# Kernel optimization log

Hardware: AMD Instinct MI355X
Metric: run time of the kernel (lower is better)

## Reference

```python
import jax, jax.numpy as jnp
import numpy as np

ALPHA = 0.2        # LeakyReLU negative slope
NEG_INF = -9e15    # mask value used by the torch module


def setup_inputs() -> dict:
    key = jax.random.key(0)
    ks = jax.random.split(key, 7)
    B, T, N, Cin = 4, 12, 1024, 64
    Fout, Em = 64, 16
    x = jax.random.normal(ks[0], (B, T, N, Cin), dtype=jnp.float32)
    adj = jax.random.randint(ks[1], (N, N), 0, 2, dtype=jnp.int32)
    emb1 = jax.random.normal(ks[2], (N, Em), dtype=jnp.float32)
    emb2 = jax.random.normal(ks[3], (N, Em), dtype=jnp.float32)
    W = jax.random.normal(ks[4], (Cin, Fout), dtype=jnp.float32) * (1.0 / np.sqrt(Cin))
    a = jax.random.normal(ks[5], (2 * Fout, 1), dtype=jnp.float32) * 0.1
    a2 = jax.random.normal(ks[6], (2 * Em, 1), dtype=jnp.float32) * 0.1
    return {"x": x, "adj": adj, "emb1": emb1, "emb2": emb2, "W": W, "a": a, "a2": a2}


def reference(x, adj, emb1, emb2, W, a, a2):
    B, T, N, Cin = x.shape
    Fout = W.shape[1]
    Em = emb1.shape[1]
    # Linear projection, fold batch*time: Wh [BT, N, Fout]
    Wh = jnp.einsum('btnc,cf->btnf', x, W).reshape(B * T, N, Fout)
    # Additive attention scores from node features
    s1 = Wh @ a[:Fout, 0]          # [BT, N]
    s2 = Wh @ a[Fout:, 0]          # [BT, N]
    e1 = s1[:, :, None] + s2[:, None, :]   # [BT, N, N]
    # Additive scores from static embeddings (shared across batch*time)
    f1 = emb1 @ a2[:Em, 0]         # [N]
    f2 = emb2 @ a2[Em:, 0]         # [N]
    e2 = f1[:, None] + f2[None, :]          # [N, N]
    e = jax.nn.leaky_relu(e1 + e2[None, :, :], negative_slope=ALPHA)
    # Adjacency mask + row softmax (dropout is inference no-op)
    att = jnp.where(adj[None, :, :] > 0, e, jnp.float32(NEG_INF))
    att = jax.nn.softmax(att, axis=-1)
    h_prime = att @ Wh                       # [BT, N, Fout]
    return jax.nn.elu(h_prime.reshape(B, T, N, Fout))
```

## Files before the change

kernel.cpp:

```cpp
#include <hip/hip_runtime.h>
#include <hip/hip_bf16.h>
#include <math.h>

#define BT 48
#define N 1024
#define F 64
#define CIN 64
#define EM 16
#define LRELU_A 0.2f
#define L2E 1.4426950408889634f

typedef short bf16x8 __attribute__((ext_vector_type(8)));
typedef float f32x4  __attribute__((ext_vector_type(4)));
typedef unsigned int u32x4 __attribute__((ext_vector_type(4)));

__device__ __forceinline__ unsigned short f2bf(float f) {
    unsigned int u = __float_as_uint(f);
    return (unsigned short)((u + 0x7FFFu + ((u >> 16) & 1u)) >> 16);
}

__global__ __launch_bounds__(256) void k_proj_misc(
    const float* __restrict__ x, const float* __restrict__ W,
    const float* __restrict__ a,
    const int* __restrict__ adj,
    const float* __restrict__ emb1, const float* __restrict__ emb2,
    const float* __restrict__ a2,
    unsigned short* __restrict__ WhSw,
    float* __restrict__ s1, float* __restrict__ s2,
    unsigned int* __restrict__ adjBits,
    float* __restrict__ f1, float* __restrict__ f2)
{
    const int tid = threadIdx.x;
    const int b   = blockIdx.x;

    __shared__ __align__(16) float sx[64 * 64];
    __shared__ __align__(16) float sWT[64 * 68];
    __shared__ __align__(16) unsigned short sT[64 * 80];

    const int bt  = b >> 4;
    const int n0  = (b & 15) * 64;
    const size_t grow = (size_t)bt * N + n0;

    {
        const float4* xv = (const float4*)(x + grow * CIN);
        float4* sxv = (float4*)sx;
        for (int i = tid; i < 64 * CIN / 4; i += 256) sxv[i] = xv[i];
        for (int i = tid; i < CIN * F; i += 256)
            sWT[(i & 63) * 68 + (i >> 6)] = W[i];
    }
    __syncthreads();

    const int f = tid & 63;
    const int w = tid >> 6;
    const float a1 = a[f], a2c = a[F + f];

    float acc[16];
#pragma unroll
    for (int t = 0; t < 16; ++t) acc[t] = 0.f;

    for (int cb = 0; cb < CIN; cb += 4) {
        const float4 wv = *(const float4*)&sWT[f * 68 + cb];
#pragma unroll
        for (int t = 0; t < 16; ++t) {
            const float4 xv = *(const float4*)&sx[(w * 16 + t) * 64 + cb];
            acc[t] = fmaf(xv.x, wv.x, acc[t]);
            acc[t] = fmaf(xv.y, wv.y, acc[t]);
            acc[t] = fmaf(xv.z, wv.z, acc[t]);
            acc[t] = fmaf(xv.w, wv.w, acc[t]);
        }
    }

#pragma unroll
    for (int t = 0; t < 16; ++t) {
        float v1 = acc[t] * a1;
        float v2 = acc[t] * a2c;
#pragma unroll
        for (int off = 32; off >= 1; off >>= 1) {
            v1 += __shfl_xor(v1, off, 64);
            v2 += __shfl_xor(v2, off, 64);
        }
        if (f == 0) {
            s1[grow + w * 16 + t] = v1;
            s2[grow + w * 16 + t] = v2;
        }
        sT[f * 80 + w * 16 + t] = f2bf(acc[t]);
    }
    __syncthreads();

    {
        const int ff = tid >> 2, q = tid & 3;
        const int slot = (q + ff) & 3;
        const int nb0 = (b & 15) * 2;
#pragma unroll
        for (int nbL = 0; nbL < 2; ++nbL) {
            const size_t dst = ((size_t)(bt * 32 + nb0 + nbL) * 64 + ff) * 32 + slot * 8;
            *(uint4*)&WhSw[dst] = *(const uint4*)&sT[ff * 80 + nbL * 32 + q * 8];
        }
    }

    if (b < 128) {
        const int idx = b * 256 + tid;
        const int r = idx >> 5, w32 = idx & 31;
        const int* p = adj + (size_t)r * N + w32 * 32;
        unsigned int m = 0;
#pragma unroll
        for (int j = 0; j < 32; ++j) m |= (p[j] > 0 ? 1u : 0u) << j;
        adjBits[idx] = m;
    } else if (b < 132) {
        const int n = (b - 128) * 256 + tid;
        float v1 = 0.f, v2 = 0.f;
#pragma unroll
        for (int k = 0; k < EM; ++k) {
            v1 = fmaf(emb1[n * EM + k], a2[k], v1);
            v2 = fmaf(emb2[n * EM + k], a2[EM + k], v2);
        }
        f1[n] = v1; f2[n] = v2;
    }
}


#define WAIT_VM4 asm volatile("s_waitcnt vmcnt(4)" ::: "memory")
#define WAIT_VM0 asm volatile("s_waitcnt vmcnt(0)" ::: "memory")
#define BAR __builtin_amdgcn_s_barrier()

#define PAIR(x1e, x1o, x2e, x2o, bit, dest) do {                           \
    float p0_ = fmaxf((x1e) * E1, (x2e) * E2);                             \
    float p1_ = fmaxf((x1o) * E1, (x2o) * E2);                             \
    p0_ = ((mb_ >> (bit)) & 1u) ? p0_ : 0.f;                               \
    p1_ = ((mb_ >> ((bit) + 1)) & 1u) ? p1_ : 0.f;                         \
    lsum += p0_ + p1_;                                                     \
    unsigned int pk_;                                                      \
    asm("v_cvt_pk_bf16_f32 %0, %1, %2" : "=v"(pk_) : "v"(p0_), "v"(p1_)); \
    dest = pk_;                                                            \
} while (0)

#define MAKE_ONE(ch, ks, Avar, abword) do {                                \
    const int jb_ = (ch) * 128 + (ks) * 32 + q * 8;                        \
    const float4 x1a_ = *(const float4*)&sX1[jb_];                         \
    const float4 x1b_ = *(const float4*)&sX1[jb_ + 4];                     \
    const float4 x2a_ = *(const float4*)&sX2[jb_];                         \
    const float4 x2b_ = *(const float4*)&sX2[jb_ + 4];                     \
    const unsigned int mb_ = ((abword) >> (q * 8)) & 0xFFu;                \
    unsigned int u0_, u1_, u2_, u3_;                                       \
    PAIR(x1a_.x, x1a_.y, x2a_.x, x2a_.y, 0, u0_);                          \
    PAIR(x1a_.z, x1a_.w, x2a_.z, x2a_.w, 2, u1_);                          \
    PAIR(x1b_.x, x1b_.y, x2b_.x, x2b_.y, 4, u2_);                          \
    PAIR(x1b_.z, x1b_.w, x2b_.z, x2b_.w, 6, u3_);                          \
    u32x4 av_; av_.x = u0_; av_.y = u1_; av_.z = u2_; av_.w = u3_;         \
    Avar = __builtin_bit_cast(bf16x8, av_);                                \
} while (0)

#define MAKE_AFR(ch, abv, A0, A1, A2, A3) do {                             \
    MAKE_ONE(ch, 0, A0, abv.x);                                            \
    MAKE_ONE(ch, 1, A1, abv.y);                                            \
    MAKE_ONE(ch, 2, A2, abv.z);                                            \
    MAKE_ONE(ch, 3, A3, abv.w);                                            \
} while (0)

#define MFMA_KS(ct, ks, Af) do {                                           \
    const bf16x8 bb_ = *(const bf16x8*)(src_ + (ks) * 4096 +               \
                        ((ct) * 16 + m15) * 64 + slotoff);                 \
    acc##ct = __builtin_amdgcn_mfma_f32_16x16x32_bf16(Af, bb_, acc##ct,    \
                                                      0, 0, 0);            \
} while (0)

#define MFMA_CT(ct, A0, A1, A2, A3) do {                                   \
    MFMA_KS(ct, 0, A0); MFMA_KS(ct, 1, A1);                                \
    MFMA_KS(ct, 2, A2); MFMA_KS(ct, 3, A3);                                \
} while (0)

#define MFMA_CHUNK(ch, A0, A1, A2, A3) do {                                \
    const char* src_ = (const char*)sB[(ch) & 1];                          \
    MFMA_CT(0, A0, A1, A2, A3); MFMA_CT(1, A0, A1, A2, A3);                \
    MFMA_CT(2, A0, A1, A2, A3); MFMA_CT(3, A0, A1, A2, A3);                \
} while (0)

#define DMA(ch) do {                                                       \
    const unsigned short* dsrc_ = gBbt + (ch) * 8192 + w * 2048 + lane * 8;\
    unsigned short* ddst_ = &sB[(ch) & 1][w * 2048];                       \
    __builtin_amdgcn_global_load_lds(                                      \
        (const __attribute__((address_space(1))) unsigned int*)(dsrc_),    \
        (__attribute__((address_space(3))) unsigned int*)(ddst_), 16, 0, 0);\
    __builtin_amdgcn_global_load_lds(                                      \
        (const __attribute__((address_space(1))) unsigned int*)(dsrc_+512),\
        (__attribute__((address_space(3))) unsigned int*)(ddst_+512), 16, 0, 0);\
    __builtin_amdgcn_global_load_lds(                                      \
        (const __attribute__((address_space(1))) unsigned int*)(dsrc_+1024),\
        (__attribute__((address_space(3))) unsigned int*)(ddst_+1024), 16, 0, 0);\
    __builtin_amdgcn_global_load_lds(                                      \
        (const __attribute__((address_space(1))) unsigned int*)(dsrc_+1536),\
        (__attribute__((address_space(3))) unsigned int*)(ddst_+1536), 16, 0, 0);\
} while (0)

#define EPI(ct, accv) do {                                                 \
    float h0_ = accv.x * rinv0, h1_ = accv.y * rinv1,                      \
          h2_ = accv.z * rinv2, h3_ = accv.w * rinv3;                      \
    h0_ = (h0_ > 0.f) ? h0_ : (__expf(h0_) - 1.f);                         \
    h1_ = (h1_ > 0.f) ? h1_ : (__expf(h1_) - 1.f);                         \
    h2_ = (h2_ > 0.f) ? h2_ : (__expf(h2_) - 1.f);                         \
    h3_ = (h3_ > 0.f) ? h3_ : (__expf(h3_) - 1.f);                         \
    float* op_ = out + (size_t)(bt * N + i0 + w * 16 + q * 4) * F          \
                 + (ct) * 16 + m15;                                        \
    op_[0 * F] = h0_; op_[1 * F] = h1_; op_[2 * F] = h2_; op_[3 * F] = h3_;\
} while (0)

__global__ __launch_bounds__(256, 3) void k_attn(
    const unsigned int* __restrict__ adjBits,
    const unsigned short* __restrict__ WhSw,
    const float* __restrict__ s1, const float* __restrict__ s2,
    const float* __restrict__ f1v, const float* __restrict__ f2v,
    float* __restrict__ out)
{
    __shared__ __align__(16) float sX1[N];
    __shared__ __align__(16) float sX2[N];
    __shared__ __align__(16) unsigned short sB[2][8192];
    __shared__ float sWmax[4];

    const int tid  = threadIdx.x;
    const int xcd = blockIdx.x & 7;
    const int idx = blockIdx.x >> 3;
    const int bt  = xcd * 6 + (idx >> 4);
    const int i0  = (idx & 15) * 64;
    const int lane = tid & 63;
    const int w    = tid >> 6;
    const int q    = lane >> 4;
    const int m15  = lane & 15;

    const int growq = i0 + w * 16 + m15;
    const unsigned int* abRow = adjBits + growq * 32;
    const uint4* abRow4 = (const uint4*)abRow;

    const uint4 ab0 = abRow4[0], ab1 = abRow4[1], ab2 = abRow4[2], ab3 = abRow4[3];
    const uint4 ab4 = abRow4[4], ab5 = abRow4[5], ab6 = abRow4[6], ab7 = abRow4[7];
    const float rraw = s1[bt * N + growq] + f1v[growq];

    float cmax = -1e30f;
    for (int j = tid; j < N; j += 256) {
        const float c = (s2[bt * N + j] + f2v[j]) * L2E;
        sX1[j] = exp2f(c);
        sX2[j] = exp2f(LRELU_A * c);
        cmax = fmaxf(cmax, c);
    }
#pragma unroll
    for (int off = 32; off >= 1; off >>= 1) cmax = fmaxf(cmax, __shfl_xor(cmax, off, 64));
    if (lane == 0) sWmax[w] = cmax;
    __syncthreads();
    const float mx = fmaxf(fmaxf(sWmax[0], sWmax[1]), fmaxf(sWmax[2], sWmax[3]));

    const float r    = rraw * L2E;
    const float smx  = r + mx;
    const float mhat = fmaxf(smx, LRELU_A * smx);
    const float E1 = exp2f(r - mhat);
    const float E2 = exp2f(LRELU_A * r - mhat);
    float lsum = 0.f;

    const unsigned short* gBbt = WhSw + (size_t)bt * 65536;
    const int slotoff = ((q + m15) & 3) * 16;

    f32x4 acc0 = 0.f, acc1 = 0.f, acc2 = 0.f, acc3 = 0.f;
    bf16x8 fA0, fA1, fA2, fA3, fB0, fB1, fB2, fB3;

    MAKE_AFR(0, ab0, fA0, fA1, fA2, fA3);
    DMA(0); DMA(1);

    WAIT_VM4; BAR;
    MFMA_CHUNK(0, fA0, fA1, fA2, fA3); MAKE_AFR(1, ab1, fB0, fB1, fB2, fB3);
    BAR; DMA(2); WAIT_VM4; BAR;
    MFMA_CHUNK(1, fB0, fB1, fB2, fB3); MAKE_AFR(2, ab2, fA0, fA1, fA2, fA3);
    BAR; DMA(3); WAIT_VM4; BAR;
    MFMA_CHUNK(2, fA0, fA1, fA2, fA3); MAKE_AFR(3, ab3, fB0, fB1, fB2, fB3);
    BAR; DMA(4); WAIT_VM4; BAR;
    MFMA_CHUNK(3, fB0, fB1, fB2, fB3); MAKE_AFR(4, ab4, fA0, fA1, fA2, fA3);
    BAR; DMA(5); WAIT_VM4; BAR;
    MFMA_CHUNK(4, fA0, fA1, fA2, fA3); MAKE_AFR(5, ab5, fB0, fB1, fB2, fB3);
    BAR; DMA(6); WAIT_VM4; BAR;
    MFMA_CHUNK(5, fB0, fB1, fB2, fB3); MAKE_AFR(6, ab6, fA0, fA1, fA2, fA3);
    BAR; DMA(7); WAIT_VM4; BAR;
    MFMA_CHUNK(6, fA0, fA1, fA2, fA3); MAKE_AFR(7, ab7, fB0, fB1, fB2, fB3);
    WAIT_VM0; BAR;
    MFMA_CHUNK(7, fB0, fB1, fB2, fB3);

    lsum += __shfl_xor(lsum, 16, 64);
    lsum += __shfl_xor(lsum, 32, 64);

    const float rinv0 = 1.f / __shfl(lsum, q * 4 + 0, 64);
    const float rinv1 = 1.f / __shfl(lsum, q * 4 + 1, 64);
    const float rinv2 = 1.f / __shfl(lsum, q * 4 + 2, 64);
    const float rinv3 = 1.f / __shfl(lsum, q * 4 + 3, 64);

    EPI(0, acc0); EPI(1, acc1); EPI(2, acc2); EPI(3, acc3);
}

extern "C" void kernel_launch(void* const* d_in, const int* in_sizes, int n_in,
                              void* d_out, int out_size, void* d_ws, size_t ws_size,
                              hipStream_t stream)
{
    const float* x    = (const float*)d_in[0];
    const int*   adj  = (const int*)  d_in[1];
    const float* emb1 = (const float*)d_in[2];
    const float* emb2 = (const float*)d_in[3];
    const float* W    = (const float*)d_in[4];
    const float* a    = (const float*)d_in[5];
    const float* a2   = (const float*)d_in[6];
    float* out = (float*)d_out;

    unsigned short* WhSw = (unsigned short*)d_ws;
    float* s1 = (float*)(WhSw + (size_t)BT * 65536);
    float* s2 = s1 + BT * N;
    float* f1 = s2 + BT * N;
    float* f2 = f1 + N;
    unsigned int* adjBits = (unsigned int*)(f2 + N);

    hipLaunchKernelGGL(k_proj_misc, dim3(768), dim3(256), 0, stream,
                       x, W, a, adj, emb1, emb2, a2, WhSw, s1, s2, adjBits, f1, f2);
    hipLaunchKernelGGL(k_attn, dim3(BT * 16), dim3(256), 0, stream,
                       adjBits, WhSw, s1, s2, f1, f2, out);
}
```

Baseline: 117.4 us.

## Fuse projection and attention kernels with a software grid barrier

```diff
diff --git a/kernel.cpp b/kernel.cpp
--- a/kernel.cpp
+++ b/kernel.cpp
@@ -9,6 +9,7 @@
 #define EM 16
 #define LRELU_A 0.2f
 #define L2E 1.4426950408889634f
+#define NBLK 768u
 
 typedef short bf16x8 __attribute__((ext_vector_type(8)));
 typedef float f32x4  __attribute__((ext_vector_type(4)));
@@ -19,104 +20,7 @@
     return (unsigned short)((u + 0x7FFFu + ((u >> 16) & 1u)) >> 16);
 }
 
-__global__ __launch_bounds__(256) void k_proj_misc(
-    const float* __restrict__ x, const float* __restrict__ W,
-    const float* __restrict__ a,
-    const int* __restrict__ adj,
-    const float* __restrict__ emb1, const float* __restrict__ emb2,
-    const float* __restrict__ a2,
-    unsigned short* __restrict__ WhSw,
-    float* __restrict__ s1, float* __restrict__ s2,
-    unsigned int* __restrict__ adjBits,
-    float* __restrict__ f1, float* __restrict__ f2)
-{
-    const int tid = threadIdx.x;
-    const int b   = blockIdx.x;
-
-    __shared__ __align__(16) float sx[64 * 64];
-    __shared__ __align__(16) float sWT[64 * 68];
-    __shared__ __align__(16) unsigned short sT[64 * 80];
-
-    const int bt  = b >> 4;
-    const int n0  = (b & 15) * 64;
-    const size_t grow = (size_t)bt * N + n0;
-
-    {
-        const float4* xv = (const float4*)(x + grow * CIN);
-        float4* sxv = (float4*)sx;
-        for (int i = tid; i < 64 * CIN / 4; i += 256) sxv[i] = xv[i];
-        for (int i = tid; i < CIN * F; i += 256)
-            sWT[(i & 63) * 68 + (i >> 6)] = W[i];
-    }
-    __syncthreads();
-
-    const int f = tid & 63;
-    const int w = tid >> 6;
-    const float a1 = a[f], a2c = a[F + f];
-
-    float acc[16];
-#pragma unroll
-    for (int t = 0; t < 16; ++t) acc[t] = 0.f;
-
-    for (int cb = 0; cb < CIN; cb += 4) {
-        const float4 wv = *(const float4*)&sWT[f * 68 + cb];
-#pragma unroll
-        for (int t = 0; t < 16; ++t) {
-            const float4 xv = *(const float4*)&sx[(w * 16 + t) * 64 + cb];
-            acc[t] = fmaf(xv.x, wv.x, acc[t]);
-            acc[t] = fmaf(xv.y, wv.y, acc[t]);
-            acc[t] = fmaf(xv.z, wv.z, acc[t]);
-            acc[t] = fmaf(xv.w, wv.w, acc[t]);
-        }
-    }
-
-#pragma unroll
-    for (int t = 0; t < 16; ++t) {
-        float v1 = acc[t] * a1;
-        float v2 = acc[t] * a2c;
-#pragma unroll
-        for (int off = 32; off >= 1; off >>= 1) {
-            v1 += __shfl_xor(v1, off, 64);
-            v2 += __shfl_xor(v2, off, 64);
-        }
-        if (f == 0) {
-            s1[grow + w * 16 + t] = v1;
-            s2[grow + w * 16 + t] = v2;
-        }
-        sT[f * 80 + w * 16 + t] = f2bf(acc[t]);
-    }
-    __syncthreads();
-
-    {
-        const int ff = tid >> 2, q = tid & 3;
-        const int slot = (q + ff) & 3;
-        const int nb0 = (b & 15) * 2;
-#pragma unroll
-        for (int nbL = 0; nbL < 2; ++nbL) {
-            const size_t dst = ((size_t)(bt * 32 + nb0 + nbL) * 64 + ff) * 32 + slot * 8;
-            *(uint4*)&WhSw[dst] = *(const uint4*)&sT[ff * 80 + nbL * 32 + q * 8];
-        }
-    }
-
-    if (b < 128) {
-        const int idx = b * 256 + tid;
-        const int r = idx >> 5, w32 = idx & 31;
-        const int* p = adj + (size_t)r * N + w32 * 32;
-        unsigned int m = 0;
-#pragma unroll
-        for (int j = 0; j < 32; ++j) m |= (p[j] > 0 ? 1u : 0u) << j;
-        adjBits[idx] = m;
-    } else if (b < 132) {
-        const int n = (b - 128) * 256 + tid;
-        float v1 = 0.f, v2 = 0.f;
-#pragma unroll
-        for (int k = 0; k < EM; ++k) {
-            v1 = fmaf(emb1[n * EM + k], a2[k], v1);
-            v2 = fmaf(emb2[n * EM + k], a2[EM + k], v2);
-        }
-        f1[n] = v1; f2[n] = v2;
-    }
-}
+__global__ void k_zero(unsigned int* bar) { if (threadIdx.x == 0) *bar = 0u; }
 
 
 #define WAIT_VM4 asm volatile("s_waitcnt vmcnt(4)" ::: "memory")
@@ -170,14 +74,14 @@
 } while (0)
 
 #define MFMA_CHUNK(ch, A0, A1, A2, A3) do {                                \
-    const char* src_ = (const char*)sB[(ch) & 1];                          \
+    const char* src_ = (const char*)(sB + ((ch) & 1) * 8192);              \
     MFMA_CT(0, A0, A1, A2, A3); MFMA_CT(1, A0, A1, A2, A3);                \
     MFMA_CT(2, A0, A1, A2, A3); MFMA_CT(3, A0, A1, A2, A3);                \
 } while (0)
 
 #define DMA(ch) do {                                                       \
     const unsigned short* dsrc_ = gBbt + (ch) * 8192 + w * 2048 + lane * 8;\
-    unsigned short* ddst_ = &sB[(ch) & 1][w * 2048];                       \
+    unsigned short* ddst_ = sB + ((ch) & 1) * 8192 + w * 2048;             \
     __builtin_amdgcn_global_load_lds(                                      \
         (const __attribute__((address_space(1))) unsigned int*)(dsrc_),    \
         (__attribute__((address_space(3))) unsigned int*)(ddst_), 16, 0, 0);\
@@ -199,96 +103,202 @@
     h1_ = (h1_ > 0.f) ? h1_ : (__expf(h1_) - 1.f);                         \
     h2_ = (h2_ > 0.f) ? h2_ : (__expf(h2_) - 1.f);                         \
     h3_ = (h3_ > 0.f) ? h3_ : (__expf(h3_) - 1.f);                         \
-    float* op_ = out + (size_t)(bt * N + i0 + w * 16 + q * 4) * F          \
+    float* op_ = out + (size_t)(bt2 * N + i0 + w * 16 + q * 4) * F         \
                  + (ct) * 16 + m15;                                        \
     op_[0 * F] = h0_; op_[1 * F] = h1_; op_[2 * F] = h2_; op_[3 * F] = h3_;\
 } while (0)
 
-__global__ __launch_bounds__(256, 3) void k_attn(
-    const unsigned int* __restrict__ adjBits,
-    const unsigned short* __restrict__ WhSw,
-    const float* __restrict__ s1, const float* __restrict__ s2,
-    const float* __restrict__ f1v, const float* __restrict__ f2v,
+__global__ __launch_bounds__(256, 3) void k_fused(
+    const float* __restrict__ x, const float* __restrict__ W,
+    const float* __restrict__ a,
+    const int* __restrict__ adj,
+    const float* __restrict__ emb1, const float* __restrict__ emb2,
+    const float* __restrict__ a2,
+    unsigned short* __restrict__ WhSw,
+    float* __restrict__ s1, float* __restrict__ s2,
+    unsigned int* __restrict__ adjBits,
+    float* __restrict__ f1, float* __restrict__ f2,
+    unsigned int* __restrict__ gbar,
     float* __restrict__ out)
 {
-    __shared__ __align__(16) float sX1[N];
-    __shared__ __align__(16) float sX2[N];
-    __shared__ __align__(16) unsigned short sB[2][8192];
-    __shared__ float sWmax[4];
-
-    const int tid  = threadIdx.x;
-    const int xcd = blockIdx.x & 7;
-    const int idx = blockIdx.x >> 3;
-    const int bt  = xcd * 6 + (idx >> 4);
-    const int i0  = (idx & 15) * 64;
+    __shared__ __align__(16) char smem[44032];
+
+    const int tid = threadIdx.x;
+    const int b   = blockIdx.x;
     const int lane = tid & 63;
     const int w    = tid >> 6;
-    const int q    = lane >> 4;
-    const int m15  = lane & 15;
-
-    const int growq = i0 + w * 16 + m15;
-    const unsigned int* abRow = adjBits + growq * 32;
-    const uint4* abRow4 = (const uint4*)abRow;
-
-    const uint4 ab0 = abRow4[0], ab1 = abRow4[1], ab2 = abRow4[2], ab3 = abRow4[3];
-    const uint4 ab4 = abRow4[4], ab5 = abRow4[5], ab6 = abRow4[6], ab7 = abRow4[7];
-    const float rraw = s1[bt * N + growq] + f1v[growq];
-
-    float cmax = -1e30f;
-    for (int j = tid; j < N; j += 256) {
-        const float c = (s2[bt * N + j] + f2v[j]) * L2E;
-        sX1[j] = exp2f(c);
-        sX2[j] = exp2f(LRELU_A * c);
-        cmax = fmaxf(cmax, c);
+
+    {
+        float* sx  = (float*)smem;
+        float* sWT = sx + 4096;
+        unsigned short* sT = (unsigned short*)(sWT + 4352);
+
+        const int bt  = b >> 4;
+        const int n0  = (b & 15) * 64;
+        const size_t grow = (size_t)bt * N + n0;
+
+        {
+            const float4* xv = (const float4*)(x + grow * CIN);
+            float4* sxv = (float4*)sx;
+            for (int i = tid; i < 64 * CIN / 4; i += 256) sxv[i] = xv[i];
+            for (int i = tid; i < CIN * F; i += 256)
+                sWT[(i & 63) * 68 + (i >> 6)] = W[i];
+        }
+        __syncthreads();
+
+        const int f = tid & 63;
+        const float a1 = a[f], a2c = a[F + f];
+
+        float acc[16];
+#pragma unroll
+        for (int t = 0; t < 16; ++t) acc[t] = 0.f;
+
+        for (int cb = 0; cb < CIN; cb += 4) {
+            const float4 wv = *(const float4*)&sWT[f * 68 + cb];
+#pragma unroll
+            for (int t = 0; t < 16; ++t) {
+                const float4 xv = *(const float4*)&sx[(w * 16 + t) * 64 + cb];
+                acc[t] = fmaf(xv.x, wv.x, acc[t]);
+                acc[t] = fmaf(xv.y, wv.y, acc[t]);
+                acc[t] = fmaf(xv.z, wv.z, acc[t]);
+                acc[t] = fmaf(xv.w, wv.w, acc[t]);
+            }
+        }
+
+#pragma unroll
+        for (int t = 0; t < 16; ++t) {
+            float v1 = acc[t] * a1;
+            float v2 = acc[t] * a2c;
+#pragma unroll
+            for (int off = 32; off >= 1; off >>= 1) {
+                v1 += __shfl_xor(v1, off, 64);
+                v2 += __shfl_xor(v2, off, 64);
+            }
+            if (f == 0) {
+                s1[grow + w * 16 + t] = v1;
+                s2[grow + w * 16 + t] = v2;
+            }
+            sT[f * 80 + w * 16 + t] = f2bf(acc[t]);
+        }
+        __syncthreads();
+
+        {
+            const int ff = tid >> 2, qq = tid & 3;
+            const int slot = (qq + ff) & 3;
+            const int nb0 = (b & 15) * 2;
+#pragma unroll
+            for (int nbL = 0; nbL < 2; ++nbL) {
+                const size_t dst = ((size_t)(bt * 32 + nb0 + nbL) * 64 + ff) * 32 + slot * 8;
+                *(uint4*)&WhSw[dst] = *(const uint4*)&sT[ff * 80 + nbL * 32 + qq * 8];
+            }
+        }
+
+        if (b < 128) {
+            const int idx = b * 256 + tid;
+            const int r = idx >> 5, w32 = idx & 31;
+            const int* p = adj + (size_t)r * N + w32 * 32;
+            unsigned int m = 0;
+#pragma unroll
+            for (int j = 0; j < 32; ++j) m |= (p[j] > 0 ? 1u : 0u) << j;
+            adjBits[idx] = m;
+        } else if (b < 132) {
+            const int n = (b - 128) * 256 + tid;
+            float v1 = 0.f, v2 = 0.f;
+#pragma unroll
+            for (int k = 0; k < EM; ++k) {
+                v1 = fmaf(emb1[n * EM + k], a2[k], v1);
+                v2 = fmaf(emb2[n * EM + k], a2[EM + k], v2);
+            }
+            f1[n] = v1; f2[n] = v2;
+        }
     }
-#pragma unroll
-    for (int off = 32; off >= 1; off >>= 1) cmax = fmaxf(cmax, __shfl_xor(cmax, off, 64));
-    if (lane == 0) sWmax[w] = cmax;
+
     __syncthreads();
-    const float mx = fmaxf(fmaxf(sWmax[0], sWmax[1]), fmaxf(sWmax[2], sWmax[3]));
-
-    const float r    = rraw * L2E;
-    const float smx  = r + mx;
-    const float mhat = fmaxf(smx, LRELU_A * smx);
-    const float E1 = exp2f(r - mhat);
-    const float E2 = exp2f(LRELU_A * r - mhat);
-    float lsum = 0.f;
-
-    const unsigned short* gBbt = WhSw + (size_t)bt * 65536;
-    const int slotoff = ((q + m15) & 3) * 16;
-
-    f32x4 acc0 = 0.f, acc1 = 0.f, acc2 = 0.f, acc3 = 0.f;
-    bf16x8 fA0, fA1, fA2, fA3, fB0, fB1, fB2, fB3;
-
-    MAKE_AFR(0, ab0, fA0, fA1, fA2, fA3);
-    DMA(0); DMA(1);
-
-    WAIT_VM4; BAR;
-    MFMA_CHUNK(0, fA0, fA1, fA2, fA3); MAKE_AFR(1, ab1, fB0, fB1, fB2, fB3);
-    BAR; DMA(2); WAIT_VM4; BAR;
-    MFMA_CHUNK(1, fB0, fB1, fB2, fB3); MAKE_AFR(2, ab2, fA0, fA1, fA2, fA3);
-    BAR; DMA(3); WAIT_VM4; BAR;
-    MFMA_CHUNK(2, fA0, fA1, fA2, fA3); MAKE_AFR(3, ab3, fB0, fB1, fB2, fB3);
-    BAR; DMA(4); WAIT_VM4; BAR;
-    MFMA_CHUNK(3, fB0, fB1, fB2, fB3); MAKE_AFR(4, ab4, fA0, fA1, fA2, fA3);
-    BAR; DMA(5); WAIT_VM4; BAR;
-    MFMA_CHUNK(4, fA0, fA1, fA2, fA3); MAKE_AFR(5, ab5, fB0, fB1, fB2, fB3);
-    BAR; DMA(6); WAIT_VM4; BAR;
-    MFMA_CHUNK(5, fB0, fB1, fB2, fB3); MAKE_AFR(6, ab6, fA0, fA1, fA2, fA3);
-    BAR; DMA(7); WAIT_VM4; BAR;
-    MFMA_CHUNK(6, fA0, fA1, fA2, fA3); MAKE_AFR(7, ab7, fB0, fB1, fB2, fB3);
-    WAIT_VM0; BAR;
-    MFMA_CHUNK(7, fB0, fB1, fB2, fB3);
-
-    lsum += __shfl_xor(lsum, 16, 64);
-    lsum += __shfl_xor(lsum, 32, 64);
-
-    const float rinv0 = 1.f / __shfl(lsum, q * 4 + 0, 64);
-    const float rinv1 = 1.f / __shfl(lsum, q * 4 + 1, 64);
-    const float rinv2 = 1.f / __shfl(lsum, q * 4 + 2, 64);
-    const float rinv3 = 1.f / __shfl(lsum, q * 4 + 3, 64);
-
-    EPI(0, acc0); EPI(1, acc1); EPI(2, acc2); EPI(3, acc3);
+    __threadfence();
+    if (tid == 0) {
+        __hip_atomic_fetch_add(gbar, 1u, __ATOMIC_ACQ_REL, __HIP_MEMORY_SCOPE_AGENT);
+        while (__hip_atomic_load(gbar, __ATOMIC_ACQUIRE, __HIP_MEMORY_SCOPE_AGENT) < NBLK)
+            __builtin_amdgcn_s_sleep(2);
+    }
+    __syncthreads();
+    __threadfence();
+
+    {
+        float* sX1 = (float*)smem;
+        float* sX2 = sX1 + 1024;
+        unsigned short* sB = (unsigned short*)(sX2 + 1024);
+        float* sWmax = (float*)(sB + 16384);
+
+        const int xcd = b & 7;
+        const int idx = b >> 3;
+        const int bt2 = xcd * 6 + (idx >> 4);
+        const int i0  = (idx & 15) * 64;
+        const int q    = lane >> 4;
+        const int m15  = lane & 15;
+
+        const int growq = i0 + w * 16 + m15;
+        const uint4* abRow4 = (const uint4*)(adjBits + (size_t)growq * 32);
+
+        const uint4 ab0 = abRow4[0], ab1 = abRow4[1], ab2 = abRow4[2], ab3 = abRow4[3];
+        const uint4 ab4 = abRow4[4], ab5 = abRow4[5], ab6 = abRow4[6], ab7 = abRow4[7];
+        const float rraw = s1[bt2 * N + growq] + f1[growq];
+
+        float cmax = -1e30f;
+        for (int j = tid; j < N; j += 256) {
+            const float c = (s2[bt2 * N + j] + f2[j]) * L2E;
+            sX1[j] = exp2f(c);
+            sX2[j] = exp2f(LRELU_A * c);
+            cmax = fmaxf(cmax, c);
+        }
+#pragma unroll
+        for (int off = 32; off >= 1; off >>= 1) cmax = fmaxf(cmax, __shfl_xor(cmax, off, 64));
+        if (lane == 0) sWmax[w] = cmax;
+        __syncthreads();
+        const float mx = fmaxf(fmaxf(sWmax[0], sWmax[1]), fmaxf(sWmax[2], sWmax[3]));
+
+        const float r    = rraw * L2E;
+        const float smx  = r + mx;
+        const float mhat = fmaxf(smx, LRELU_A * smx);
+        const float E1 = exp2f(r - mhat);
+        const float E2 = exp2f(LRELU_A * r - mhat);
+        float lsum = 0.f;
+
+        const unsigned short* gBbt = WhSw + (size_t)bt2 * 65536;
+        const int slotoff = ((q + m15) & 3) * 16;
+
+        f32x4 acc0 = 0.f, acc1 = 0.f, acc2 = 0.f, acc3 = 0.f;
+        bf16x8 fA0, fA1, fA2, fA3, fB0, fB1, fB2, fB3;
+
+        MAKE_AFR(0, ab0, fA0, fA1, fA2, fA3);
+        DMA(0); DMA(1);
+
+        WAIT_VM4; BAR;
+        MFMA_CHUNK(0, fA0, fA1, fA2, fA3); MAKE_AFR(1, ab1, fB0, fB1, fB2, fB3);
+        BAR; DMA(2); WAIT_VM4; BAR;
+        MFMA_CHUNK(1, fB0, fB1, fB2, fB3); MAKE_AFR(2, ab2, fA0, fA1, fA2, fA3);
+        BAR; DMA(3); WAIT_VM4; BAR;
+        MFMA_CHUNK(2, fA0, fA1, fA2, fA3); MAKE_AFR(3, ab3, fB0, fB1, fB2, fB3);
+        BAR; DMA(4); WAIT_VM4; BAR;
+        MFMA_CHUNK(3, fB0, fB1, fB2, fB3); MAKE_AFR(4, ab4, fA0, fA1, fA2, fA3);
+        BAR; DMA(5); WAIT_VM4; BAR;
+        MFMA_CHUNK(4, fA0, fA1, fA2, fA3); MAKE_AFR(5, ab5, fB0, fB1, fB2, fB3);
+        BAR; DMA(6); WAIT_VM4; BAR;
+        MFMA_CHUNK(5, fB0, fB1, fB2, fB3); MAKE_AFR(6, ab6, fA0, fA1, fA2, fA3);
+        BAR; DMA(7); WAIT_VM4; BAR;
+        MFMA_CHUNK(6, fA0, fA1, fA2, fA3); MAKE_AFR(7, ab7, fB0, fB1, fB2, fB3);
+        WAIT_VM0; BAR;
+        MFMA_CHUNK(7, fB0, fB1, fB2, fB3);
+
+        lsum += __shfl_xor(lsum, 16, 64);
+        lsum += __shfl_xor(lsum, 32, 64);
+
+        const float rinv0 = 1.f / __shfl(lsum, q * 4 + 0, 64);
+        const float rinv1 = 1.f / __shfl(lsum, q * 4 + 1, 64);
+        const float rinv2 = 1.f / __shfl(lsum, q * 4 + 2, 64);
+        const float rinv3 = 1.f / __shfl(lsum, q * 4 + 3, 64);
+
+        EPI(0, acc0); EPI(1, acc1); EPI(2, acc2); EPI(3, acc3);
+    }
 }
 
 extern "C" void kernel_launch(void* const* d_in, const int* in_sizes, int n_in,
@@ -310,9 +320,10 @@
     float* f1 = s2 + BT * N;
     float* f2 = f1 + N;
     unsigned int* adjBits = (unsigned int*)(f2 + N);
-
-    hipLaunchKernelGGL(k_proj_misc, dim3(768), dim3(256), 0, stream,
-                       x, W, a, adj, emb1, emb2, a2, WhSw, s1, s2, adjBits, f1, f2);
-    hipLaunchKernelGGL(k_attn, dim3(BT * 16), dim3(256), 0, stream,
-                       adjBits, WhSw, s1, s2, f1, f2, out);
+    unsigned int* gbar = adjBits + 32768;
+
+    hipLaunchKernelGGL(k_zero, dim3(1), dim3(64), 0, stream, gbar);
+    hipLaunchKernelGGL(k_fused, dim3(NBLK), dim3(256), 0, stream,
+                       x, W, a, adj, emb1, emb2, a2, WhSw, s1, s2,
+                       adjBits, f1, f2, gbar, out);
 }
```

New measurement: 269.4 us. 2.3x slower.
